# Kernel tuning notes

Measured on AMD Instinct MI355X. Metric: run time of the kernel, lower is better.

The kernel has to match this reference:

```python
import jax, jax.numpy as jnp
import numpy as np

PRED_LEN = 12
A = 128          # agents in the single scene
NHEAD = 8
NLAYERS = 2
D = 256          # embedding_dim
MLP = 1024
HDIM = 128       # decoder_h_dim
OBS_LEN = 8
MEMLEN = A * OBS_LEN
NEG = -1e9       # stands in for float('-inf') in the AR mask


def _sinusoid(length, d):
    pos = jnp.arange(length, dtype=jnp.float32)[:, None]
    div = jnp.exp(jnp.arange(0, d, 2, dtype=jnp.float32) * (-np.log(10000.0) / d))
    ang = pos * div
    pe = jnp.zeros((length, d), jnp.float32)
    pe = pe.at[:, 0::2].set(jnp.sin(ang))
    pe = pe.at[:, 1::2].set(jnp.cos(ang))
    return pe


def _ln(x, g, b):
    m = x.mean(-1, keepdims=True)
    v = ((x - m) ** 2).mean(-1, keepdims=True)
    return (x - m) / jnp.sqrt(v + 1e-5) * g + b


def _mha(q, k, v, Wq, bq, Wk, bk, Wv, bv, Wo, bo, mask):
    dh = D // NHEAD
    qh = (q @ Wq.T + bq).reshape(-1, NHEAD, dh)
    kh = (k @ Wk.T + bk).reshape(-1, NHEAD, dh)
    vh = (v @ Wv.T + bv).reshape(-1, NHEAD, dh)
    s = jnp.einsum('ihd,jhd->hij', qh, kh) / np.sqrt(dh) + mask[None]
    w = jax.nn.softmax(s, axis=-1)
    o = jnp.einsum('hij,jhd->ihd', w, vh).reshape(-1, D)
    return o @ Wo.T + bo


def _forward(last_pos, decoder_state, memory, agent_mask, in_W, in_b, out_W, out_b,
             sa_Wq, sa_bq, sa_Wk, sa_bk, sa_Wv, sa_bv, sa_Wo, sa_bo,
             ca_Wq, ca_bq, ca_Wk, ca_bk, ca_Wv, ca_bv, ca_Wo, ca_bo,
             ff_W1, ff_b1, ff_W2, ff_b2,
             ln1_g, ln1_b, ln2_g, ln2_b, ln3_g, ln3_b):
    agent_pe = _sinusoid(A, D)
    scene_pos = last_pos
    tokens = []
    outs = []
    for s in range(PRED_LEN):  # fixed-length AR loop (unrolled, static shapes)
        feat = jnp.concatenate([scene_pos, decoder_state], axis=-1)  # [A, 2+HDIM]
        tokens.append(feat @ in_W.T + in_b)                          # [A, D]
        steps = s + 1
        tgt = jnp.concatenate(tokens, axis=0)                        # [steps*A, D]
        time_enc = jnp.repeat(_sinusoid(steps, D), A, axis=0)
        x = tgt + time_enc + jnp.tile(agent_pe, (steps, 1))
        times = jnp.repeat(jnp.arange(steps), A)
        # generate_ar_mask: block-causal over time, tiled agent_mask within block
        tgt_mask = jnp.where(times[None, :] > times[:, None], NEG,
                             jnp.tile(agent_mask, (steps, steps)))
        # generate_mask: tiled agent_mask for cross-attention to memory
        mem_mask = jnp.tile(agent_mask, (steps, MEMLEN // A))
        for l in range(NLAYERS):
            sa = _mha(x, x, x, sa_Wq[l], sa_bq[l], sa_Wk[l], sa_bk[l],
                      sa_Wv[l], sa_bv[l], sa_Wo[l], sa_bo[l], tgt_mask)
            x = _ln(x + sa, ln1_g[l], ln1_b[l])
            ca = _mha(x, memory, memory, ca_Wq[l], ca_bq[l], ca_Wk[l], ca_bk[l],
                      ca_Wv[l], ca_bv[l], ca_Wo[l], ca_bo[l], mem_mask)
            x = _ln(x + ca, ln2_g[l], ln2_b[l])
            ff = jax.nn.relu(x @ ff_W1[l].T + ff_b1[l]) @ ff_W2[l].T + ff_b2[l]
            x = _ln(x + ff, ln3_g[l], ln3_b[l])
        rel = x[-A:] @ out_W.T + out_b                               # [A, 2]
        outs.append(rel)
        scene_pos = scene_pos + rel
    return jnp.stack(outs, axis=0)                                   # [PRED_LEN, A, 2]


def setup_inputs():
    key = jax.random.key(0)
    ks = jax.random.split(key, 40)
    def rn(k, shape, scale=0.02):
        return jax.random.normal(k, shape, jnp.float32) * scale
    inp = {
        'last_pos': jax.random.normal(ks[0], (A, 2), jnp.float32),
        'decoder_state': jax.random.normal(ks[1], (A, HDIM), jnp.float32),
        'memory': jax.random.normal(ks[2], (MEMLEN, D), jnp.float32),
        'agent_mask': jnp.zeros((A, A), jnp.float32),
        'in_W': rn(ks[3], (D, 2 + HDIM)),
        'in_b': jnp.zeros((D,), jnp.float32),
        'out_W': rn(ks[4], (2, D)),
        'out_b': jnp.zeros((2,), jnp.float32),
    }
    names = ['sa_Wq', 'sa_Wk', 'sa_Wv', 'sa_Wo', 'ca_Wq', 'ca_Wk', 'ca_Wv', 'ca_Wo']
    for i, n in enumerate(names):
        inp[n] = rn(ks[5 + i], (NLAYERS, D, D))
        inp[n.replace('W', 'b')] = jnp.zeros((NLAYERS, D), jnp.float32)
    inp['ff_W1'] = rn(ks[20], (NLAYERS, MLP, D))
    inp['ff_b1'] = jnp.zeros((NLAYERS, MLP), jnp.float32)
    inp['ff_W2'] = rn(ks[21], (NLAYERS, D, MLP))
    inp['ff_b2'] = jnp.zeros((NLAYERS, D), jnp.float32)
    for n in ['ln1', 'ln2', 'ln3']:
        inp[n + '_g'] = jnp.ones((NLAYERS, D), jnp.float32)
        inp[n + '_b'] = jnp.zeros((NLAYERS, D), jnp.float32)
    return inp


def reference(last_pos, decoder_state, memory, agent_mask, in_W, in_b, out_W, out_b,
              sa_Wq, sa_bq, sa_Wk, sa_bk, sa_Wv, sa_bv, sa_Wo, sa_bo,
              ca_Wq, ca_bq, ca_Wk, ca_bk, ca_Wv, ca_bv, ca_Wo, ca_bo,
              ff_W1, ff_b1, ff_W2, ff_b2,
              ln1_g, ln1_b, ln2_g, ln2_b, ln3_g, ln3_b):
    return _forward(last_pos, decoder_state, memory, agent_mask, in_W, in_b, out_W, out_b,
                    sa_Wq, sa_bq, sa_Wk, sa_bk, sa_Wv, sa_bv, sa_Wo, sa_bo,
                    ca_Wq, ca_bq, ca_Wk, ca_bk, ca_Wv, ca_bv, ca_Wo, ca_bo,
                    ff_W1, ff_b1, ff_W2, ff_b2,
                    ln1_g, ln1_b, ln2_g, ln2_b, ln3_g, ln3_b)
```

## Files before the change

### kernel.cpp

```cpp
#include <hip/hip_runtime.h>
#include <math.h>

#define AGENTS 128
#define DIM 256
#define MEM_LEN 1024
#define PRED 12
#define MAXS (PRED * AGENTS)
#define NWG 32

typedef __attribute__((ext_vector_type(8))) short short8;
typedef __attribute__((ext_vector_type(4))) float f32x4;

#define MFMA(a, b, c) __builtin_amdgcn_mfma_f32_16x16x32_bf16(a, b, c, 0, 0, 0)

__device__ __forceinline__ unsigned short f2bf(float f) {
  union { float f; unsigned u; } v; v.f = f;
  unsigned r = v.u + 0x7fffu + ((v.u >> 16) & 1u);
  return (unsigned short)(r >> 16);
}
__device__ __forceinline__ float bfval(unsigned short b) {
  union { unsigned u; float f; } v; v.u = (unsigned)b << 16; return v.f;
}
__device__ __forceinline__ short8 afrag8(const float* p) {
  float4 a = *(const float4*)p;
  float4 b = *(const float4*)(p + 4);
  short8 r;
  r[0] = (short)f2bf(a.x); r[1] = (short)f2bf(a.y);
  r[2] = (short)f2bf(a.z); r[3] = (short)f2bf(a.w);
  r[4] = (short)f2bf(b.x); r[5] = (short)f2bf(b.y);
  r[6] = (short)f2bf(b.z); r[7] = (short)f2bf(b.w);
  return r;
}

__device__ __forceinline__ void ln_stats(const float* __restrict__ pst, int row,
                                         float& mean, float& rstd) {
  float4 p0 = *(const float4*)(pst + row * 8);
  float4 p1 = *(const float4*)(pst + row * 8 + 4);
  float s  = p0.x + p0.z + p1.x + p1.z;
  float ss = p0.y + p0.w + p1.y + p1.w;
  mean = s * (1.0f / 256.0f);
  rstd = rsqrtf(ss * (1.0f / 256.0f) - mean * mean + 1e-5f);
}

__device__ __forceinline__ short8 afragLN(const float* __restrict__ yr,
                                          const float* __restrict__ lg,
                                          const float* __restrict__ lb,
                                          int k, float mean, float rstd) {
  float4 a = *(const float4*)(yr + k), b = *(const float4*)(yr + k + 4);
  float4 ga = *(const float4*)(lg + k), gb = *(const float4*)(lg + k + 4);
  float4 ba = *(const float4*)(lb + k), bb = *(const float4*)(lb + k + 4);
  short8 r;
  r[0] = (short)f2bf((a.x - mean) * rstd * ga.x + ba.x);
  r[1] = (short)f2bf((a.y - mean) * rstd * ga.y + ba.y);
  r[2] = (short)f2bf((a.z - mean) * rstd * ga.z + ba.z);
  r[3] = (short)f2bf((a.w - mean) * rstd * ga.w + ba.w);
  r[4] = (short)f2bf((b.x - mean) * rstd * gb.x + bb.x);
  r[5] = (short)f2bf((b.y - mean) * rstd * gb.y + bb.y);
  r[6] = (short)f2bf((b.z - mean) * rstd * gb.z + bb.z);
  r[7] = (short)f2bf((b.w - mean) * rstd * gb.w + bb.w);
  return r;
}

struct MegaP {
  const float *last_pos, *ds, *mask;
  const float *in_b, *out_W, *out_b;
  const float *sa_bq, *sa_bk, *sa_bv, *sa_bo;
  const float *ca_bq, *ca_bo;
  const float *ff_b1, *ff_b2;
  const float *ln1_g, *ln1_b, *ln2_g, *ln2_b, *ln3_g, *ln3_b;
  float *out;
  const float *peA, *peT;
  float *x0rot;
  unsigned short *xb0rot;
  unsigned short *qrot, *abufrot, *cabufrot;
  float *Y1rot, *Y2rot, *Y3rot;
  float *pst1rot, *pst2rot, *pst3rot;
  unsigned short *midrot;
  unsigned short *saK, *saV;
  const unsigned short *memK, *memV;
  const unsigned short *dxdb, *ffW1b, *ffW2b, *inWb;
  unsigned *barCnt;
};

__device__ __forceinline__ void gridbar(unsigned* cnt, unsigned& tgt) {
  __syncthreads();
  tgt += NWG;
  if (threadIdx.x == 0) {
    unsigned old = __hip_atomic_fetch_add(cnt, 1u, __ATOMIC_RELEASE,
                                          __HIP_MEMORY_SCOPE_AGENT);
    if (old + 1u < tgt) {
      while (__hip_atomic_load(cnt, __ATOMIC_RELAXED,
                               __HIP_MEMORY_SCOPE_AGENT) < tgt)
        __builtin_amdgcn_s_sleep(1);
    }
  }
  __syncthreads();
  asm volatile("" ::: "memory");
}

__device__ __forceinline__ void score_tile(short8 kf, short8 qf, const float* m4,
                                           unsigned short* dst, float& lsum) {
  const float scale = 0.17677669529663687f;
  f32x4 zz = {};
  f32x4 sc = MFMA(kf, qf, zz);
  unsigned short b0 = f2bf(__expf(sc[0] * scale + m4[0]));
  unsigned short b1 = f2bf(__expf(sc[1] * scale + m4[1]));
  unsigned short b2 = f2bf(__expf(sc[2] * scale + m4[2]));
  unsigned short b3 = f2bf(__expf(sc[3] * scale + m4[3]));
  lsum += bfval(b0) + bfval(b1) + bfval(b2) + bfval(b3);
  uint2 u2;
  u2.x = (unsigned)b0 | ((unsigned)b1 << 16);
  u2.y = (unsigned)b2 | ((unsigned)b3 << 16);
  *(uint2*)dst = u2;
}

__device__ __forceinline__ void flash64(const unsigned short* __restrict__ kh,
                                        const unsigned short* __restrict__ vbase,
                                        int hcol, short8 qf, const float mk[2][4][4],
                                        int S, unsigned short* psrow,
                                        int c15, int g8, int g,
                                        float& lsum, f32x4& oa0, f32x4& oa1) {
  for (int kc = 0; kc < S; kc += 64) {
    const int pp = (kc >> 6) & 1;
#pragma unroll
    for (int t = 0; t < 4; ++t) {
      short8 kf = *(const short8*)(kh + (kc + t * 16 + c15) * 32 + g8);
      score_tile(kf, qf, mk[pp][t], psrow + t * 16 + g * 4, lsum);
    }
#pragma unroll
    for (int ks = 0; ks < 2; ++ks) {
      short8 pf = *(const short8*)(psrow + ks * 32 + g8);
      int j = kc + ks * 32 + g8;
      const unsigned short* vb = vbase + (j >> 4) * 4096 + (j & 15);
      short8 v0 = *(const short8*)(vb + (hcol + c15) * 16);
      short8 v1 = *(const short8*)(vb + (hcol + c15 + 16) * 16);
      oa0 = MFMA(v0, pf, oa0);
      oa1 = MFMA(v1, pf, oa1);
    }
  }
}

__device__ void ph_embed(const MegaP& p, int wg, int s, float (*sscene)[2]) {
  if (wg >= 8) return;
  const int tid = threadIdx.x;
  const int rb = wg >> 2, cb = wg & 3;
  if (s > 0) {
    if (tid < 128) {
      const int lrow = tid >> 1, j = tid & 1;
      const int row = rb * 64 + lrow;
      const int rotp = s * 2 - 1;
      float mean, rstd;
      ln_stats(p.pst3rot + rotp * 1024, row, mean, rstd);
      const float* yr = p.Y3rot + rotp * 32768 + row * 256;
      const float* wr = p.out_W + j * 256;
      const float* g3 = p.ln3_g + 256;
      const float* b3 = p.ln3_b + 256;
      float a = 0.f;
      for (int k = 0; k < 256; k += 4) {
        float4 y = *(const float4*)(yr + k);
        float4 gg = *(const float4*)(g3 + k);
        float4 bb = *(const float4*)(b3 + k);
        float4 ww = *(const float4*)(wr + k);
        a += ((y.x - mean) * rstd * gg.x + bb.x) * ww.x
           + ((y.y - mean) * rstd * gg.y + bb.y) * ww.y
           + ((y.z - mean) * rstd * gg.z + bb.z) * ww.z
           + ((y.w - mean) * rstd * gg.w + bb.w) * ww.w;
      }
      a += p.out_b[j];
      if (cb == 0) p.out[((s - 1) * AGENTS + row) * 2 + j] = a;
      sscene[lrow][j] += a;
    }
  } else {
    if (tid < 128)
      sscene[tid >> 1][tid & 1] = p.last_pos[(rb * 64 + (tid >> 1)) * 2 + (tid & 1)];
  }
  __syncthreads();
  if (s == PRED) return;

  const int l = tid & 63, w = tid >> 6;
  const int c15 = l & 15, g8 = (l >> 4) * 8, r0v = (l >> 4) * 4;
  const int rowb = rb * 64 + w * 16;
  const int arow = rowb + c15;
  const int lsrow = w * 16 + c15;
  const int colb = cb * 64;
  f32x4 acc[4] = {};
  const unsigned short* wp = p.inWb + (colb + c15) * 160 + g8;
  for (int kc = 0; kc < 5; ++kc) {
    short8 af;
#pragma unroll
    for (int j = 0; j < 8; ++j) {
      int kk = kc * 32 + g8 + j;
      float v = (kk < 2) ? sscene[lsrow][kk]
                         : ((kk < 130) ? p.ds[arow * 128 + (kk - 2)] : 0.f);
      af[j] = (short)f2bf(v);
    }
#pragma unroll
    for (int t = 0; t < 4; ++t)
      acc[t] = MFMA(af, *(const short8*)(wp + t * 16 * 160 + kc * 32), acc[t]);
  }
  float* x0 = p.x0rot + s * 32768;
  unsigned short* xb0 = p.xb0rot + s * 32768;
#pragma unroll
  for (int t = 0; t < 4; ++t) {
    const int col = colb + t * 16 + c15;
    const float bb = p.in_b[col] + p.peT[s * DIM + col];
#pragma unroll
    for (int r = 0; r < 4; ++r) {
      const int row = rowb + r0v + r;
      float v = acc[t][r] + bb + p.peA[row * DIM + col];
      x0[row * DIM + col] = v;
      xb0[row * DIM + col] = f2bf(v);
    }
  }
}

__device__ void ph_qkv(const MegaP& p, int wg, int s, int li) {
  if (wg >= 24) return;
  const int which = wg >> 3, t8 = wg & 7;
  const int rb = t8 >> 2, cb = t8 & 3;
  const int tid = threadIdx.x, l = tid & 63, w = tid >> 6;
  const int c15 = l & 15, g8 = (l >> 4) * 8, r0v = (l >> 4) * 4;
  const int rowb = rb * 64 + w * 16;
  const int arow = rowb + c15;
  const int colb = cb * 64;
  const int rot = s * 2 + li;

  const unsigned short* ab = p.xb0rot + s * 32768;
  const float* Ya = p.Y3rot + (rot - 1) * 32768;
  float mean = 0.f, rstd = 0.f;
  if (li == 1) ln_stats(p.pst3rot + (rot - 1) * 1024, arow, mean, rstd);

  const unsigned short* W = p.dxdb + which * 131072 + li * 65536;
  const float* bias = (which == 0 ? p.sa_bq : (which == 1 ? p.sa_bk : p.sa_bv)) + li * 256;

  f32x4 acc[4] = {};
  const unsigned short* wp = W + (colb + c15) * 256 + g8;
  for (int kc = 0; kc < 8; ++kc) {
    short8 af = (li == 0) ? *(const short8*)(ab + arow * 256 + kc * 32 + g8)
                          : afragLN(Ya + arow * 256, p.ln3_g, p.ln3_b,
                                    kc * 32 + g8, mean, rstd);
#pragma unroll
    for (int t = 0; t < 4; ++t)
      acc[t] = MFMA(af, *(const short8*)(wp + t * 16 * 256 + kc * 32), acc[t]);
  }

  if (which == 0) {
    unsigned short* qdst = p.qrot + rot * 32768;
#pragma unroll
    for (int t = 0; t < 4; ++t) {
      int col = colb + t * 16 + c15;
      float bb = bias[col];
#pragma unroll
      for (int r = 0; r < 4; ++r)
        qdst[(rowb + r0v + r) * 256 + col] = f2bf(acc[t][r] + bb);
    }
  } else if (which == 1) {
    unsigned short* Ko = p.saK + li * 393216;
#pragma unroll
    for (int t = 0; t < 4; ++t) {
      int col = colb + t * 16 + c15;
      float bb = bias[col];
      int hh = col >> 5, d = col & 31;
#pragma unroll
      for (int r = 0; r < 4; ++r)
        Ko[hh * (MAXS * 32) + (s * 128 + rowb + r0v + r) * 32 + d] = f2bf(acc[t][r] + bb);
    }
  } else {
    unsigned short* Vo = p.saV + li * 393216;
    const int kb = s * 8 + rb * 4 + w;
#pragma unroll
    for (int t = 0; t < 4; ++t) {
      int col = colb + t * 16 + c15;
      float bb = bias[col];
      unsigned long long pk = 0;
#pragma unroll
      for (int r = 0; r < 4; ++r)
        pk |= (unsigned long long)f2bf(acc[t][r] + bb) << (16 * r);
      *(unsigned long long*)&Vo[(kb * 256 + col) * 16 + r0v] = pk;
    }
  }
}

__device__ void ph_attn_sa(const MegaP& p, unsigned short (*ps)[16][96],
                           int wg, int s, int li) {
  if (wg >= 16) return;
  const int rb = wg >> 3, h = wg & 7;
  const int tid = threadIdx.x, l = tid & 63, w = tid >> 6;
  const int c15 = l & 15, g = l >> 4, g8 = g * 8;
  const int rot = s * 2 + li;
  const int qrow = rb * 64 + w * 16 + c15;
  const int S = (s + 1) * 128;

  short8 qf = *(const short8*)(p.qrot + rot * 32768 + qrow * 256 + h * 32 + g8);
  float mk[2][4][4];
#pragma unroll
  for (int pp = 0; pp < 2; ++pp)
#pragma unroll
    for (int t = 0; t < 4; ++t)
#pragma unroll
      for (int r = 0; r < 4; ++r)
        mk[pp][t][r] = p.mask[qrow * AGENTS + pp * 64 + t * 16 + g * 4 + r];

  f32x4 oa0 = {}, oa1 = {};
  float lsum = 0.f;
  flash64(p.saK + li * 393216 + h * (MAXS * 32), p.saV + li * 393216,
          h * 32, qf, mk, S, &ps[w][c15][0], c15, g8, g, lsum, oa0, oa1);
  lsum += __shfl_xor(lsum, 16, 64);
  lsum += __shfl_xor(lsum, 32, 64);
  const float inv = 1.0f / lsum;
  unsigned long long pk0 = 0, pk1 = 0;
#pragma unroll
  for (int r = 0; r < 4; ++r) {
    pk0 |= (unsigned long long)f2bf(oa0[r] * inv) << (16 * r);
    pk1 |= (unsigned long long)f2bf(oa1[r] * inv) << (16 * r);
  }
  unsigned short* adst = p.abufrot + rot * 32768;
  *(unsigned long long*)(adst + h * 4096 + qrow * 32 + g * 4) = pk0;
  *(unsigned long long*)(adst + h * 4096 + qrow * 32 + 16 + g * 4) = pk1;
}

__device__ void ph_attn_ca(const MegaP& p, unsigned short (*sq)[16][32],
                           unsigned short (*ps)[16][96], int wg, int s, int li) {
  if (wg >= 16) return;
  const int rb = wg >> 3, h = wg & 7;
  const int tid = threadIdx.x, l = tid & 63, w = tid >> 6;
  const int c15 = l & 15, g = l >> 4, g8 = g * 8, r0v = g * 4;
  const int rot = s * 2 + li;
  const int rowb = rb * 64 + w * 16;
  const int arow = rowb + c15;

  const float* Ya = p.Y1rot + rot * 32768;
  const float* lga = p.ln1_g + li * 256;
  const float* lba = p.ln1_b + li * 256;
  float mean, rstd;
  ln_stats(p.pst1rot + rot * 1024, arow, mean, rstd);

  const unsigned short* Wq = p.dxdb + 4 * 131072 + li * 65536;
  const float* bq = p.ca_bq + li * 256;
  f32x4 q0 = {}, q1 = {};
  const unsigned short* wp = Wq + (h * 32 + c15) * 256 + g8;
  for (int kc = 0; kc < 8; ++kc) {
    short8 af = afragLN(Ya + arow * 256, lga, lba, kc * 32 + g8, mean, rstd);
    q0 = MFMA(af, *(const short8*)(wp + kc * 32), q0);
    q1 = MFMA(af, *(const short8*)(wp + 16 * 256 + kc * 32), q1);
  }
  {
    const float b0 = bq[h * 32 + c15], b1 = bq[h * 32 + 16 + c15];
#pragma unroll
    for (int r = 0; r < 4; ++r) {
      sq[w][r0v + r][c15]      = f2bf(q0[r] + b0);
      sq[w][r0v + r][16 + c15] = f2bf(q1[r] + b1);
    }
  }
  short8 qf = *(const short8*)&sq[w][c15][g8];

  float mk[2][4][4];
#pragma unroll
  for (int pp = 0; pp < 2; ++pp)
#pragma unroll
    for (int t = 0; t < 4; ++t)
#pragma unroll
      for (int r = 0; r < 4; ++r)
        mk[pp][t][r] = p.mask[arow * AGENTS + pp * 64 + t * 16 + g * 4 + r];

  f32x4 oa0 = {}, oa1 = {};
  float lsum = 0.f;
  flash64(p.memK + li * 262144 + h * (MEM_LEN * 32), p.memV + li * 262144,
          h * 32, qf, mk, MEM_LEN, &ps[w][c15][0], c15, g8, g, lsum, oa0, oa1);
  lsum += __shfl_xor(lsum, 16, 64);
  lsum += __shfl_xor(lsum, 32, 64);
  const float inv = 1.0f / lsum;
  unsigned long long pk0 = 0, pk1 = 0;
#pragma unroll
  for (int r = 0; r < 4; ++r) {
    pk0 |= (unsigned long long)f2bf(oa0[r] * inv) << (16 * r);
    pk1 |= (unsigned long long)f2bf(oa1[r] * inv) << (16 * r);
  }
  unsigned short* adst = p.cabufrot + rot * 32768;
  *(unsigned long long*)(adst + h * 4096 + arow * 32 + g * 4) = pk0;
  *(unsigned long long*)(adst + h * 4096 + arow * 32 + 16 + g * 4) = pk1;
}

template <int ALAY, int RES>
__device__ void ph_oproj(const MegaP& p, int wg,
    const unsigned short* __restrict__ ab,
    const unsigned short* __restrict__ W, const float* __restrict__ bias,
    const float* __restrict__ res,
    const float* __restrict__ Yp, const float* __restrict__ pstp,
    const float* __restrict__ gp, const float* __restrict__ bp,
    float* __restrict__ Yo, float* __restrict__ psto)
{
  if (wg >= 8) return;
  const int tid = threadIdx.x, l = tid & 63, w = tid >> 6;
  const int c15 = l & 15, g8 = (l >> 4) * 8, r0v = (l >> 4) * 4;
  const int rowb = (wg >> 2) * 64 + w * 16;
  const int arow = rowb + c15;
  const int cb = wg & 3, colb = cb * 64;
  constexpr int K = ALAY ? 1024 : 256;

  f32x4 acc[4] = {};
  const unsigned short* wp = W + (colb + c15) * K + g8;
  for (int kc = 0; kc < K / 32; ++kc) {
    short8 af;
    if (ALAY == 0) af = *(const short8*)(ab + kc * 4096 + arow * 32 + g8);
    else           af = *(const short8*)(ab + arow * 1024 + kc * 32 + g8);
#pragma unroll
    for (int t = 0; t < 4; ++t)
      acc[t] = MFMA(af, *(const short8*)(wp + t * 16 * K + kc * 32), acc[t]);
  }

  float mp[4], rp[4];
  if (RES == 2) {
#pragma unroll
    for (int r = 0; r < 4; ++r) ln_stats(pstp, rowb + r0v + r, mp[r], rp[r]);
  }
  float v[4][4];
#pragma unroll
  for (int t = 0; t < 4; ++t) {
    const int col = colb + t * 16 + c15;
    const float bb = bias[col];
    float gpp = 0.f, bpp = 0.f;
    if (RES == 2) { gpp = gp[col]; bpp = bp[col]; }
#pragma unroll
    for (int r = 0; r < 4; ++r) {
      const int row = rowb + r0v + r;
      float x = acc[t][r] + bb;
      if (RES == 1) x += res[row * 256 + col];
      if (RES == 2) x += (Yp[row * 256 + col] - mp[r]) * rp[r] * gpp + bpp;
      Yo[row * 256 + col] = x;
      v[t][r] = x;
    }
  }
#pragma unroll
  for (int r = 0; r < 4; ++r) {
    float s  = v[0][r] + v[1][r] + v[2][r] + v[3][r];
    float ss = v[0][r]*v[0][r] + v[1][r]*v[1][r] + v[2][r]*v[2][r] + v[3][r]*v[3][r];
#pragma unroll
    for (int m = 1; m < 16; m <<= 1) {
      s  += __shfl_xor(s, m, 64);
      ss += __shfl_xor(ss, m, 64);
    }
    if (c15 == 0) {
      const int row = rowb + r0v + r;
      psto[row * 8 + cb * 2]     = s;
      psto[row * 8 + cb * 2 + 1] = ss;
    }
  }
}

__device__ void ph_ff1(const MegaP& p, int wg, int s, int li) {
  const int rb = wg >> 4, cb = wg & 15;
  const int tid = threadIdx.x, l = tid & 63, w = tid >> 6;
  const int c15 = l & 15, g8 = (l >> 4) * 8, r0v = (l >> 4) * 4;
  const int rowb = rb * 64 + w * 16;
  const int arow = rowb + c15;
  const int colb = cb * 64;
  const int rot = s * 2 + li;

  const float* Ya = p.Y2rot + rot * 32768;
  const float* lga = p.ln2_g + li * 256;
  const float* lba = p.ln2_b + li * 256;
  float mean, rstd;
  ln_stats(p.pst2rot + rot * 1024, arow, mean, rstd);

  const unsigned short* W1 = p.ffW1b + li * 262144;
  const float* b1 = p.ff_b1 + li * 1024;
  f32x4 acc[4] = {};
  const unsigned short* wp = W1 + (colb + c15) * 256 + g8;
  for (int kc = 0; kc < 8; ++kc) {
    short8 af = afragLN(Ya + arow * 256, lga, lba, kc * 32 + g8, mean, rstd);
#pragma unroll
    for (int t = 0; t < 4; ++t)
      acc[t] = MFMA(af, *(const short8*)(wp + t * 16 * 256 + kc * 32), acc[t]);
  }
  unsigned short* mid = p.midrot + rot * 131072;
#pragma unroll
  for (int t = 0; t < 4; ++t) {
    const int col = colb + t * 16 + c15;
    const float bb = b1[col];
#pragma unroll
    for (int r = 0; r < 4; ++r)
      mid[(rowb + r0v + r) * 1024 + col] = f2bf(fmaxf(acc[t][r] + bb, 0.f));
  }
}

__global__ __launch_bounds__(256, 1) void mega_k(MegaP p) {
  __shared__ float sscene[64][2];
  __shared__ unsigned short sq[4][16][32];
  __shared__ unsigned short ps[4][16][96];
  const int wg = blockIdx.x;
  unsigned tgt = 0;
#define GB gridbar(p.barCnt, tgt)

  for (int s = 0; s < PRED; ++s) {
    ph_embed(p, wg, s, sscene);
    GB;
    for (int li = 0; li < 2; ++li) {
      const int rot = s * 2 + li;
      ph_qkv(p, wg, s, li);
      GB;
      ph_attn_sa(p, ps, wg, s, li);
      GB;
      if (li == 0)
        ph_oproj<0, 1>(p, wg, p.abufrot + rot * 32768,
                       p.dxdb + 3 * 131072, p.sa_bo,
                       p.x0rot + s * 32768, nullptr, nullptr, nullptr, nullptr,
                       p.Y1rot + rot * 32768, p.pst1rot + rot * 1024);
      else
        ph_oproj<0, 2>(p, wg, p.abufrot + rot * 32768,
                       p.dxdb + 3 * 131072 + 65536, p.sa_bo + 256,
                       nullptr, p.Y3rot + (rot - 1) * 32768,
                       p.pst3rot + (rot - 1) * 1024, p.ln3_g, p.ln3_b,
                       p.Y1rot + rot * 32768, p.pst1rot + rot * 1024);
      GB;
      ph_attn_ca(p, sq, ps, wg, s, li);
      GB;
      ph_oproj<0, 2>(p, wg, p.cabufrot + rot * 32768,
                     p.dxdb + 7 * 131072 + li * 65536, p.ca_bo + li * 256,
                     nullptr, p.Y1rot + rot * 32768, p.pst1rot + rot * 1024,
                     p.ln1_g + li * 256, p.ln1_b + li * 256,
                     p.Y2rot + rot * 32768, p.pst2rot + rot * 1024);
      GB;
      ph_ff1(p, wg, s, li);
      GB;
      ph_oproj<1, 2>(p, wg, p.midrot + rot * 131072,
                     p.ffW2b + li * 262144, p.ff_b2 + li * 256,
                     nullptr, p.Y2rot + rot * 32768, p.pst2rot + rot * 1024,
                     p.ln2_g + li * 256, p.ln2_b + li * 256,
                     p.Y3rot + rot * 32768, p.pst3rot + rot * 1024);
      GB;
    }
  }
  ph_embed(p, wg, PRED, sscene);
#undef GB
}

__global__ void cvt8_k(const float* p0, const float* p1, const float* p2,
                       const float* p3, const float* p4, const float* p5,
                       const float* p6, const float* p7, unsigned short* dst)
{
  const float* s;
  switch (blockIdx.z) {
    case 0: s = p0; break; case 1: s = p1; break;
    case 2: s = p2; break; case 3: s = p3; break;
    case 4: s = p4; break; case 5: s = p5; break;
    case 6: s = p6; break; default: s = p7; break;
  }
  int i = blockIdx.x * 256 + threadIdx.x;
  dst[blockIdx.z * 131072 + i] = f2bf(s[i]);
}

__global__ void cvtff_k(const float* w1, const float* w2, unsigned short* dst)
{
  const float* s = blockIdx.z ? w2 : w1;
  int i = blockIdx.x * 256 + threadIdx.x;
  dst[blockIdx.z * 524288 + i] = f2bf(s[i]);
}

__global__ void cvtinw_k(const float* w, unsigned short* dst)
{
  int i = blockIdx.x * 256 + threadIdx.x;
  if (i >= 256 * 160) return;
  int n = i / 160, k = i - n * 160;
  dst[i] = (k < 130) ? f2bf(w[n * 130 + k]) : (unsigned short)0;
}

__global__ void pe_k(float* peA, float* peT)
{
  int i = blockIdx.x * 256 + threadIdx.x;
  if (i < 128 * 256) {
    int row = i >> 8, c = i & 255, pp = c >> 1;
    float dv = expf((float)(2 * pp) * (-9.210340371976184f / 256.f));
    float ang = (float)row * dv;
    peA[i] = (c & 1) ? cosf(ang) : sinf(ang);
  } else if (i < 140 * 256) {
    int j = i - 32768;
    int s = j >> 8, c = j & 255, pp = c >> 1;
    float dv = expf((float)(2 * pp) * (-9.210340371976184f / 256.f));
    float ang = (float)s * dv;
    peT[j] = (c & 1) ? cosf(ang) : sinf(ang);
  }
}

__global__ __launch_bounds__(256) void memkv_k(
    const float* __restrict__ mem, const unsigned short* __restrict__ dxd,
    const float* __restrict__ bk, const float* __restrict__ bvv,
    unsigned short* __restrict__ memK, unsigned short* __restrict__ memV)
{
  const int li = blockIdx.z;
  const int y = blockIdx.y;
  const bool isK = y < 4;
  const int colb = (y & 3) * 64;
  const unsigned short* W = dxd + (isK ? 5 : 6) * 131072 + li * 65536;
  const float* bias = (isK ? bk : bvv) + li * 256;
  unsigned short* Ko = memK + li * 262144;
  unsigned short* Vo = memV + li * 262144;
  const int tid = threadIdx.x, l = tid & 63, w = tid >> 6;
  const int c15 = l & 15, g8 = (l >> 4) * 8, r0v = (l >> 4) * 4;
  const int rowb = blockIdx.x * 64 + w * 16;
  const int arow = rowb + c15;
  f32x4 acc[4] = {};
  const unsigned short* wp = W + (colb + c15) * 256 + g8;
  for (int kc = 0; kc < 8; ++kc) {
    short8 af = afrag8(mem + arow * 256 + kc * 32 + g8);
#pragma unroll
    for (int t = 0; t < 4; ++t)
      acc[t] = MFMA(af, *(const short8*)(wp + t * 16 * 256 + kc * 32), acc[t]);
  }
  const int kb = blockIdx.x * 4 + w;
#pragma unroll
  for (int t = 0; t < 4; ++t) {
    const int col = colb + t * 16 + c15;
    const float bb = bias[col];
    if (isK) {
      const int hh = col >> 5, d = col & 31;
#pragma unroll
      for (int r = 0; r < 4; ++r)
        Ko[hh * (MEM_LEN * 32) + (rowb + r0v + r) * 32 + d] = f2bf(acc[t][r] + bb);
    } else {
      unsigned long long pk = 0;
#pragma unroll
      for (int r = 0; r < 4; ++r)
        pk |= (unsigned long long)f2bf(acc[t][r] + bb) << (16 * r);
      *(unsigned long long*)&Vo[(kb * 256 + col) * 16 + r0v] = pk;
    }
  }
}

__global__ void initbar_k(unsigned* b) { b[0] = 0; }

extern "C" void kernel_launch(void* const* d_in, const int* in_sizes, int n_in,
                              void* d_out, int out_size, void* d_ws, size_t ws_size,
                              hipStream_t stream)
{
  float* ws = (float*)d_ws;
  float* peA = ws;
  float* peT = peA + 32768;
  float* x0rot = peT + 3072;
  float* Y1rot = x0rot + 393216;
  float* Y2rot = Y1rot + 786432;
  float* Y3rot = Y2rot + 786432;
  float* pst1rot = Y3rot + 786432;
  float* pst2rot = pst1rot + 24576;
  float* pst3rot = pst2rot + 24576;
  unsigned short* xb0rot = (unsigned short*)(pst3rot + 24576);
  unsigned short* qrot = xb0rot + 393216;
  unsigned short* abufrot = qrot + 786432;
  unsigned short* cabufrot = abufrot + 786432;
  unsigned short* midrot = cabufrot + 786432;
  unsigned short* saK = midrot + 3145728;
  unsigned short* saV = saK + 786432;
  unsigned short* memK = saV + 786432;
  unsigned short* memV = memK + 524288;
  unsigned short* dxdb = memV + 524288;
  unsigned short* ffW1b = dxdb + 1048576;
  unsigned short* ffW2b = ffW1b + 524288;
  unsigned short* inWb = ffW2b + 524288;
  unsigned* bar = (unsigned*)(inWb + 40960);

  const dim3 blk(256);

  cvt8_k<<<dim3(512, 1, 8), blk, 0, stream>>>(
      (const float*)d_in[8], (const float*)d_in[10], (const float*)d_in[12],
      (const float*)d_in[14], (const float*)d_in[16], (const float*)d_in[18],
      (const float*)d_in[20], (const float*)d_in[22], dxdb);
  cvtff_k<<<dim3(2048, 1, 2), blk, 0, stream>>>((const float*)d_in[24],
                                                (const float*)d_in[26], ffW1b);
  cvtinw_k<<<160, blk, 0, stream>>>((const float*)d_in[4], inWb);
  pe_k<<<140, blk, 0, stream>>>(peA, peT);
  memkv_k<<<dim3(16, 8, 2), blk, 0, stream>>>((const float*)d_in[2], dxdb,
      (const float*)d_in[19], (const float*)d_in[21], memK, memV);
  initbar_k<<<1, 1, 0, stream>>>(bar);

  MegaP p;
  p.last_pos = (const float*)d_in[0];
  p.ds = (const float*)d_in[1];
  p.mask = (const float*)d_in[3];
  p.in_b = (const float*)d_in[5];
  p.out_W = (const float*)d_in[6];
  p.out_b = (const float*)d_in[7];
  p.sa_bq = (const float*)d_in[9];  p.sa_bk = (const float*)d_in[11];
  p.sa_bv = (const float*)d_in[13]; p.sa_bo = (const float*)d_in[15];
  p.ca_bq = (const float*)d_in[17]; p.ca_bo = (const float*)d_in[23];
  p.ff_b1 = (const float*)d_in[25]; p.ff_b2 = (const float*)d_in[27];
  p.ln1_g = (const float*)d_in[28]; p.ln1_b = (const float*)d_in[29];
  p.ln2_g = (const float*)d_in[30]; p.ln2_b = (const float*)d_in[31];
  p.ln3_g = (const float*)d_in[32]; p.ln3_b = (const float*)d_in[33];
  p.out = (float*)d_out;
  p.peA = peA; p.peT = peT;
  p.x0rot = x0rot; p.xb0rot = xb0rot;
  p.qrot = qrot; p.abufrot = abufrot; p.cabufrot = cabufrot;
  p.Y1rot = Y1rot; p.Y2rot = Y2rot; p.Y3rot = Y3rot;
  p.pst1rot = pst1rot; p.pst2rot = pst2rot; p.pst3rot = pst3rot;
  p.midrot = midrot;
  p.saK = saK; p.saV = saV; p.memK = memK; p.memV = memV;
  p.dxdb = dxdb; p.ffW1b = ffW1b; p.ffW2b = ffW2b; p.inWb = inWb;
  p.barCnt = bar;

  mega_k<<<dim3(NWG), blk, 0, stream>>>(p);
}
```

Baseline: 3.085 ms.

## Halve persistent workgroups, fuse K/V projection, use relaxed atomic stores for barriers

Cuts the persistent megakernel grid from 32 to 16 workgroups, which makes each grid barrier cheaper because fewer groups must arrive. To keep every group busy, the K and V projections are computed together in one group and each FF1 group covers twice as many columns. Inter-phase writes become relaxed agent-scope atomic stores and the barrier's fetch_add drops its release ordering, which removes fence cost. The risk is less parallelism per phase and weaker memory ordering guarantees across the barrier.

```diff
diff --git a/kernel.cpp b/kernel.cpp
--- a/kernel.cpp
+++ b/kernel.cpp
@@ -6,7 +6,7 @@
 #define MEM_LEN 1024
 #define PRED 12
 #define MAXS (PRED * AGENTS)
-#define NWG 32
+#define NWG 16
 
 typedef __attribute__((ext_vector_type(8))) short short8;
 typedef __attribute__((ext_vector_type(4))) float f32x4;
@@ -30,6 +30,11 @@
   r[4] = (short)f2bf(b.x); r[5] = (short)f2bf(b.y);
   r[6] = (short)f2bf(b.z); r[7] = (short)f2bf(b.w);
   return r;
+}
+
+template <typename T>
+__device__ __forceinline__ void ast(T* p, T v) {
+  __hip_atomic_store(p, v, __ATOMIC_RELAXED, __HIP_MEMORY_SCOPE_AGENT);
 }
 
 __device__ __forceinline__ void ln_stats(const float* __restrict__ pst, int row,
@@ -86,7 +91,7 @@
   __syncthreads();
   tgt += NWG;
   if (threadIdx.x == 0) {
-    unsigned old = __hip_atomic_fetch_add(cnt, 1u, __ATOMIC_RELEASE,
+    unsigned old = __hip_atomic_fetch_add(cnt, 1u, __ATOMIC_RELAXED,
                                           __HIP_MEMORY_SCOPE_AGENT);
     if (old + 1u < tgt) {
       while (__hip_atomic_load(cnt, __ATOMIC_RELAXED,
@@ -208,15 +213,15 @@
     for (int r = 0; r < 4; ++r) {
       const int row = rowb + r0v + r;
       float v = acc[t][r] + bb + p.peA[row * DIM + col];
-      x0[row * DIM + col] = v;
-      xb0[row * DIM + col] = f2bf(v);
+      ast(&x0[row * DIM + col], v);
+      ast(&xb0[row * DIM + col], f2bf(v));
     }
   }
 }
 
 __device__ void ph_qkv(const MegaP& p, int wg, int s, int li) {
-  if (wg >= 24) return;
-  const int which = wg >> 3, t8 = wg & 7;
+  const bool isQ = wg < 8;
+  const int t8 = isQ ? wg : (wg - 8);
   const int rb = t8 >> 2, cb = t8 & 3;
   const int tid = threadIdx.x, l = tid & 63, w = tid >> 6;
   const int c15 = l & 15, g8 = (l >> 4) * 8, r0v = (l >> 4) * 4;
@@ -230,21 +235,23 @@
   float mean = 0.f, rstd = 0.f;
   if (li == 1) ln_stats(p.pst3rot + (rot - 1) * 1024, arow, mean, rstd);
 
-  const unsigned short* W = p.dxdb + which * 131072 + li * 65536;
-  const float* bias = (which == 0 ? p.sa_bq : (which == 1 ? p.sa_bk : p.sa_bv)) + li * 256;
-
-  f32x4 acc[4] = {};
-  const unsigned short* wp = W + (colb + c15) * 256 + g8;
-  for (int kc = 0; kc < 8; ++kc) {
-    short8 af = (li == 0) ? *(const short8*)(ab + arow * 256 + kc * 32 + g8)
-                          : afragLN(Ya + arow * 256, p.ln3_g, p.ln3_b,
-                                    kc * 32 + g8, mean, rstd);
-#pragma unroll
-    for (int t = 0; t < 4; ++t)
-      acc[t] = MFMA(af, *(const short8*)(wp + t * 16 * 256 + kc * 32), acc[t]);
-  }
-
-  if (which == 0) {
+  short8 af[8];
+#pragma unroll
+  for (int kc = 0; kc < 8; ++kc)
+    af[kc] = (li == 0) ? *(const short8*)(ab + arow * 256 + kc * 32 + g8)
+                       : afragLN(Ya + arow * 256, p.ln3_g, p.ln3_b,
+                                 kc * 32 + g8, mean, rstd);
+
+  if (isQ) {
+    const unsigned short* W = p.dxdb + li * 65536;
+    const float* bias = p.sa_bq + li * 256;
+    f32x4 acc[4] = {};
+    const unsigned short* wp = W + (colb + c15) * 256 + g8;
+#pragma unroll
+    for (int kc = 0; kc < 8; ++kc)
+#pragma unroll
+      for (int t = 0; t < 4; ++t)
+        acc[t] = MFMA(af[kc], *(const short8*)(wp + t * 16 * 256 + kc * 32), acc[t]);
     unsigned short* qdst = p.qrot + rot * 32768;
 #pragma unroll
     for (int t = 0; t < 4; ++t) {
@@ -252,38 +259,46 @@
       float bb = bias[col];
 #pragma unroll
       for (int r = 0; r < 4; ++r)
-        qdst[(rowb + r0v + r) * 256 + col] = f2bf(acc[t][r] + bb);
-    }
-  } else if (which == 1) {
+        ast(&qdst[(rowb + r0v + r) * 256 + col], f2bf(acc[t][r] + bb));
+    }
+  } else {
+    const unsigned short* Wk = p.dxdb + 1 * 131072 + li * 65536;
+    const unsigned short* Wv = p.dxdb + 2 * 131072 + li * 65536;
+    const float* bk = p.sa_bk + li * 256;
+    const float* bv = p.sa_bv + li * 256;
+    f32x4 ak[4] = {}, av[4] = {};
+    const unsigned short* wpk = Wk + (colb + c15) * 256 + g8;
+    const unsigned short* wpv = Wv + (colb + c15) * 256 + g8;
+#pragma unroll
+    for (int kc = 0; kc < 8; ++kc)
+#pragma unroll
+      for (int t = 0; t < 4; ++t) {
+        ak[t] = MFMA(af[kc], *(const short8*)(wpk + t * 16 * 256 + kc * 32), ak[t]);
+        av[t] = MFMA(af[kc], *(const short8*)(wpv + t * 16 * 256 + kc * 32), av[t]);
+      }
     unsigned short* Ko = p.saK + li * 393216;
+    unsigned short* Vo = p.saV + li * 393216;
+    const int kb = s * 8 + rb * 4 + w;
 #pragma unroll
     for (int t = 0; t < 4; ++t) {
       int col = colb + t * 16 + c15;
-      float bb = bias[col];
+      float bbk = bk[col], bbv = bv[col];
       int hh = col >> 5, d = col & 31;
 #pragma unroll
       for (int r = 0; r < 4; ++r)
-        Ko[hh * (MAXS * 32) + (s * 128 + rowb + r0v + r) * 32 + d] = f2bf(acc[t][r] + bb);
-    }
-  } else {
-    unsigned short* Vo = p.saV + li * 393216;
-    const int kb = s * 8 + rb * 4 + w;
-#pragma unroll
-    for (int t = 0; t < 4; ++t) {
-      int col = colb + t * 16 + c15;
-      float bb = bias[col];
+        ast(&Ko[hh * (MAXS * 32) + (s * 128 + rowb + r0v + r) * 32 + d],
+            f2bf(ak[t][r] + bbk));
       unsigned long long pk = 0;
 #pragma unroll
       for (int r = 0; r < 4; ++r)
-        pk |= (unsigned long long)f2bf(acc[t][r] + bb) << (16 * r);
-      *(unsigned long long*)&Vo[(kb * 256 + col) * 16 + r0v] = pk;
+        pk |= (unsigned long long)f2bf(av[t][r] + bbv) << (16 * r);
+      ast((unsigned long long*)&Vo[(kb * 256 + col) * 16 + r0v], pk);
     }
   }
 }
 
 __device__ void ph_attn_sa(const MegaP& p, unsigned short (*ps)[16][96],
                            int wg, int s, int li) {
-  if (wg >= 16) return;
   const int rb = wg >> 3, h = wg & 7;
   const int tid = threadIdx.x, l = tid & 63, w = tid >> 6;
   const int c15 = l & 15, g = l >> 4, g8 = g * 8;
@@ -315,13 +330,12 @@
     pk1 |= (unsigned long long)f2bf(oa1[r] * inv) << (16 * r);
   }
   unsigned short* adst = p.abufrot + rot * 32768;
-  *(unsigned long long*)(adst + h * 4096 + qrow * 32 + g * 4) = pk0;
-  *(unsigned long long*)(adst + h * 4096 + qrow * 32 + 16 + g * 4) = pk1;
+  ast((unsigned long long*)(adst + h * 4096 + qrow * 32 + g * 4), pk0);
+  ast((unsigned long long*)(adst + h * 4096 + qrow * 32 + 16 + g * 4), pk1);
 }
 
 __device__ void ph_attn_ca(const MegaP& p, unsigned short (*sq)[16][32],
                            unsigned short (*ps)[16][96], int wg, int s, int li) {
-  if (wg >= 16) return;
   const int rb = wg >> 3, h = wg & 7;
   const int tid = threadIdx.x, l = tid & 63, w = tid >> 6;
   const int c15 = l & 15, g = l >> 4, g8 = g * 8, r0v = g * 4;
@@ -377,8 +391,8 @@
     pk1 |= (unsigned long long)f2bf(oa1[r] * inv) << (16 * r);
   }
   unsigned short* adst = p.cabufrot + rot * 32768;
-  *(unsigned long long*)(adst + h * 4096 + arow * 32 + g * 4) = pk0;
-  *(unsigned long long*)(adst + h * 4096 + arow * 32 + 16 + g * 4) = pk1;
+  ast((unsigned long long*)(adst + h * 4096 + arow * 32 + g * 4), pk0);
+  ast((unsigned long long*)(adst + h * 4096 + arow * 32 + 16 + g * 4), pk1);
 }
 
 template <int ALAY, int RES>
@@ -427,7 +441,7 @@
       float x = acc[t][r] + bb;
       if (RES == 1) x += res[row * 256 + col];
       if (RES == 2) x += (Yp[row * 256 + col] - mp[r]) * rp[r] * gpp + bpp;
-      Yo[row * 256 + col] = x;
+      ast(&Yo[row * 256 + col], x);
       v[t][r] = x;
     }
   }
@@ -442,19 +456,19 @@
     }
     if (c15 == 0) {
       const int row = rowb + r0v + r;
-      psto[row * 8 + cb * 2]     = s;
-      psto[row * 8 + cb * 2 + 1] = ss;
+      ast(&psto[row * 8 + cb * 2], s);
+      ast(&psto[row * 8 + cb * 2 + 1], ss);
     }
   }
 }
 
 __device__ void ph_ff1(const MegaP& p, int wg, int s, int li) {
-  const int rb = wg >> 4, cb = wg & 15;
+  const int rb = wg >> 3, cb = wg & 7;
   const int tid = threadIdx.x, l = tid & 63, w = tid >> 6;
   const int c15 = l & 15, g8 = (l >> 4) * 8, r0v = (l >> 4) * 4;
   const int rowb = rb * 64 + w * 16;
   const int arow = rowb + c15;
-  const int colb = cb * 64;
+  const int colb = cb * 128;
   const int rot = s * 2 + li;
 
   const float* Ya = p.Y2rot + rot * 32768;
@@ -465,22 +479,22 @@
 
   const unsigned short* W1 = p.ffW1b + li * 262144;
   const float* b1 = p.ff_b1 + li * 1024;
-  f32x4 acc[4] = {};
+  f32x4 acc[8] = {};
   const unsigned short* wp = W1 + (colb + c15) * 256 + g8;
   for (int kc = 0; kc < 8; ++kc) {
     short8 af = afragLN(Ya + arow * 256, lga, lba, kc * 32 + g8, mean, rstd);
 #pragma unroll
-    for (int t = 0; t < 4; ++t)
+    for (int t = 0; t < 8; ++t)
       acc[t] = MFMA(af, *(const short8*)(wp + t * 16 * 256 + kc * 32), acc[t]);
   }
   unsigned short* mid = p.midrot + rot * 131072;
 #pragma unroll
-  for (int t = 0; t < 4; ++t) {
+  for (int t = 0; t < 8; ++t) {
     const int col = colb + t * 16 + c15;
     const float bb = b1[col];
 #pragma unroll
     for (int r = 0; r < 4; ++r)
-      mid[(rowb + r0v + r) * 1024 + col] = f2bf(fmaxf(acc[t][r] + bb, 0.f));
+      ast(&mid[(rowb + r0v + r) * 1024 + col], f2bf(fmaxf(acc[t][r] + bb, 0.f)));
   }
 }
 
```

After: 3.590 ms. 1.16x slower.
